# Optimization experiments

Hardware: AMD Instinct MI355X
Metric: run time of the kernel (lower is better)

The kernel has to match this reference:

```python
import jax, jax.numpy as jnp
import numpy as np

K = 4096
N = 11008
GROUP_SIZE = 128
NUM_GROUPS = K // GROUP_SIZE
BATCH = 4
SEQ = 2048


def setup_inputs() -> dict:
    key = jax.random.key(0)
    kx, kw, ks = jax.random.split(key, 3)
    x = jax.random.normal(kx, (BATCH, SEQ, K), dtype=jnp.float16)
    # packed uint8 bytes, each holding two INT4 values (stored as int32)
    weight_packed = jax.random.randint(kw, (N, K // 2), 0, 256, dtype=jnp.int32)
    # positive group-wise scales ~ abs(randn)*0.1 -> uniform*0.1 is fine statistically
    scales = (jax.random.uniform(ks, (N, NUM_GROUPS), dtype=jnp.float32) * 0.1).astype(jnp.float16)
    return {"x": x, "weight_packed": weight_packed, "scales": scales}


def _dequantize(weight_packed, scales):
    # unpack: low nibble first, then high nibble -> (N, K) values in [0, 15]
    low = weight_packed & 15
    high = (weight_packed >> 4) & 15
    w_int = jnp.stack([low, high], axis=-1).reshape(weight_packed.shape[0], -1)  # (N, K)
    # symmetric dequant with implicit zero-point 8, group-wise scales
    scales_expanded = jnp.repeat(scales, GROUP_SIZE, axis=1)  # (N, K)
    return scales_expanded * (w_int.astype(jnp.float16) - jnp.float16(8.0))


def reference(x, weight_packed, scales):
    # Y = X @ W_dequant.T : (B, S, K) x (N, K) -> (B, S, N)
    w_dequant = _dequantize(weight_packed, scales)  # (N, K) fp16
    out = jnp.einsum('bsk,nk->bsn', x, w_dequant)
    return out.astype(jnp.float16)
```

## Files before the change

kernel.cpp:

```cpp
#include <hip/hip_runtime.h>
#include <stdint.h>


namespace {

typedef unsigned int u32;
typedef unsigned short u16;
typedef __attribute__((ext_vector_type(8))) short bf16x8;
typedef __attribute__((ext_vector_type(4))) float f32x4;
typedef __attribute__((ext_vector_type(4))) u32 u32x4;

constexpr int Mt = 8192;
constexpr int Nt = 11008;
constexpr int Kt = 4096;
constexpr int KP = Kt / 2;
constexpr int NG = 32;
constexpr int BM = 256;
constexpr int BN = 128;
constexpr int BK = 64;
constexpr int THREADS = 512;
constexpr int GRID = (Mt / BM) * (Nt / BN);
constexpr int NKT = Kt / BK;
constexpr int NB_CNT = Nt / BN;

__device__ __forceinline__ u16 f2bf(float f) {
  u32 u = __float_as_uint(f);
  return (u16)((u + 0x7FFFu + ((u >> 16) & 1u)) >> 16);
}
__device__ __forceinline__ u32 pk2bf(float a, float b) {
  return (u32)f2bf(a) | ((u32)f2bf(b) << 16);
}
__device__ __forceinline__ u32 dqpair(u32 b, float s, float c) {
  float f0 = (float)(b & 15u);
  float f1 = (float)((b >> 4) & 15u);
  return pk2bf(fmaf(f0, s, c), fmaf(f1, s, c));
}
__device__ __forceinline__ void async16(const void* g, void* l) {
  __builtin_amdgcn_global_load_lds(
      (const __attribute__((address_space(1))) u32*)g,
      (__attribute__((address_space(3))) u32*)l, 16, 0, 0);
}

__global__ __launch_bounds__(256) void cvt_x(const float* __restrict__ X,
                                             u32* __restrict__ O) {
  const int total = Mt * Kt / 4;
  for (int j = blockIdx.x * 256 + threadIdx.x; j < total;
       j += (int)(gridDim.x * 256)) {
    float4 v = ((const float4*)X)[j];
    ((uint2*)O)[j] = make_uint2(pk2bf(v.x, v.y), pk2bf(v.z, v.w));
  }
}

__global__ __launch_bounds__(256) void cvt_w(const int* __restrict__ W,
                                             const float* __restrict__ S,
                                             u32* __restrict__ O) {
  const int total = Nt * KP / 4;
  for (int j = blockIdx.x * 256 + threadIdx.x; j < total;
       j += (int)(gridDim.x * 256)) {
    int4 v = ((const int4*)W)[j];
    int vv[4] = {v.x, v.y, v.z, v.w};
    const int j0 = j * 4;
    const int row = j0 >> 11;
    const int jj = j0 & 2047;
    const float* sr = S + (size_t)row * NG;
    u32x4 o;
    #pragma unroll
    for (int e = 0; e < 4; ++e) {
      float s = sr[(jj + e) >> 6];
      o[e] = dqpair((u32)vv[e], s, -8.f * s);
    }
    ((u32x4*)O)[j] = o;
  }
}

template <bool PRE>
__global__ __launch_bounds__(THREADS) void gemm(
    const float* __restrict__ Xf, const int* __restrict__ W,
    const float* __restrict__ S, const u16* __restrict__ Xb,
    const u16* __restrict__ Wb, float* __restrict__ Y) {
  __shared__ __align__(16) unsigned char Alds[BM * BK * 2];
  __shared__ __align__(16) unsigned char Blds[BN * BK * 2];

  const int tid = (int)threadIdx.x;
  const int lane = tid & 63;
  const int wid = tid >> 6;
  const int wm = wid >> 1;
  const int wn = wid & 1;

  const int bid = (int)blockIdx.x;
  const int wg = (bid & 7) * (GRID / 8) + (bid >> 3);
  const int mb = wg / NB_CNT;
  const int nb = wg - mb * NB_CNT;
  const int m0 = mb * BM;
  const int n0 = nb * BN;

  const int frow = lane & 15;
  const int fk = lane >> 4;
  const int fswz = (lane & 7) << 4;
  const unsigned char* aRd = Alds + (wm * 64 + frow) * 128;
  const unsigned char* bRd = Blds + (wn * 64 + frow) * 128;

  f32x4 acc[4][4];
  #pragma unroll
  for (int i = 0; i < 4; ++i)
    #pragma unroll
    for (int j = 0; j < 4; ++j) acc[i][j] = f32x4{0.f, 0.f, 0.f, 0.f};

  const int lrow = lane >> 3, lslot = lane & 7;
  const int psl = lslot ^ (lrow & 7);
  const u16* aG = PRE ? Xb + (size_t)(m0 + wid * 32 + lrow) * Kt + psl * 8 : nullptr;
  const u16* bG = PRE ? Wb + (size_t)(n0 + wid * 16 + lrow) * Kt + psl * 8 : nullptr;
  unsigned char* aL = Alds + (wid * 32) * 128;
  unsigned char* bL = Blds + (wid * 16) * 128;

  const int arow = tid >> 3, acol = tid & 7;
  const float* fA = PRE ? nullptr : Xf + (size_t)(m0 + arow) * Kt + acol * 8;
  unsigned char* fAD = Alds + arow * 128 + ((acol ^ (arow & 7)) << 4);
  const int nloc = tid >> 3, c4 = tid & 7;
  const int* fB0 = PRE ? nullptr : W + (size_t)(n0 + nloc) * KP + c4 * 4;
  const int* fB1 = PRE ? nullptr : fB0 + (size_t)64 * KP;
  const float* sp0 = PRE ? nullptr : S + (size_t)(n0 + nloc) * NG;
  const float* sp1 = PRE ? nullptr : sp0 + (size_t)64 * NG;
  unsigned char* fBD0 = Blds + nloc * 128 + ((c4 ^ (nloc & 7)) << 4);
  unsigned char* fBD1 = fBD0 + 64 * 128;

  #pragma unroll 1
  for (int kt = 0; kt < NKT; ++kt) {
    const int k0 = kt * BK;

    if constexpr (PRE) {
      #pragma unroll
      for (int i = 0; i < 4; ++i) async16(aG + (size_t)i * 8 * Kt + k0, aL + i * 1024);
      #pragma unroll
      for (int j = 0; j < 2; ++j) async16(bG + (size_t)j * 8 * Kt + k0, bL + j * 1024);
    } else {
      #pragma unroll
      for (int p = 0; p < 4; ++p) {
        float4 x0 = *(const float4*)(fA + (size_t)p * 64 * Kt + k0);
        float4 x1 = *(const float4*)(fA + (size_t)p * 64 * Kt + k0 + 4);
        u32x4 q;
        q[0] = pk2bf(x0.x, x0.y); q[1] = pk2bf(x0.z, x0.w);
        q[2] = pk2bf(x1.x, x1.y); q[3] = pk2bf(x1.z, x1.w);
        *(u32x4*)(fAD + p * 64 * 128) = q;
      }
      const int g = k0 >> 7;
      const float s0 = sp0[g], s1 = sp1[g];
      const float c0 = -8.f * s0, c1 = -8.f * s1;
      const int4 w0 = *(const int4*)(fB0 + (k0 >> 1));
      const int4 w1 = *(const int4*)(fB1 + (k0 >> 1));
      u32x4 q0, q1;
      q0[0] = dqpair((u32)w0.x, s0, c0); q0[1] = dqpair((u32)w0.y, s0, c0);
      q0[2] = dqpair((u32)w0.z, s0, c0); q0[3] = dqpair((u32)w0.w, s0, c0);
      q1[0] = dqpair((u32)w1.x, s1, c1); q1[1] = dqpair((u32)w1.y, s1, c1);
      q1[2] = dqpair((u32)w1.z, s1, c1); q1[3] = dqpair((u32)w1.w, s1, c1);
      *(u32x4*)fBD0 = q0;
      *(u32x4*)fBD1 = q1;
    }

    __syncthreads();

    #pragma unroll
    for (int kk = 0; kk < 2; ++kk) {
      const int koff = (kk * 64 + fk * 16) ^ fswz;
      bf16x8 af[4], bfr[4];
      #pragma unroll
      for (int fm = 0; fm < 4; ++fm)
        af[fm] = *(const bf16x8*)(aRd + fm * 16 * 128 + koff);
      #pragma unroll
      for (int fn = 0; fn < 4; ++fn)
        bfr[fn] = *(const bf16x8*)(bRd + fn * 16 * 128 + koff);
      #pragma unroll
      for (int fm = 0; fm < 4; ++fm)
        #pragma unroll
        for (int fn = 0; fn < 4; ++fn)
          acc[fm][fn] = __builtin_amdgcn_mfma_f32_16x16x32_bf16(
              af[fm], bfr[fn], acc[fm][fn], 0, 0, 0);
    }

    __syncthreads();
  }

  #pragma unroll
  for (int fm = 0; fm < 4; ++fm) {
    #pragma unroll
    for (int r = 0; r < 4; ++r) {
      const size_t mrow = (size_t)(m0 + wm * 64 + fm * 16 + fk * 4 + r) * Nt;
      #pragma unroll
      for (int fn = 0; fn < 4; ++fn) {
        Y[mrow + (size_t)(n0 + wn * 64 + fn * 16 + frow)] = acc[fm][fn][r];
      }
    }
  }
}

}

extern "C" void kernel_launch(void* const* d_in, const int* in_sizes, int n_in,
                              void* d_out, int out_size, void* d_ws, size_t ws_size,
                              hipStream_t stream) {
  (void)in_sizes; (void)n_in; (void)out_size;
  const float* X = (const float*)d_in[0];
  const int* W   = (const int*)d_in[1];
  const float* S = (const float*)d_in[2];
  float* Y       = (float*)d_out;

  const size_t xbytes = (size_t)Mt * Kt * 2;
  const size_t wbytes = (size_t)Nt * Kt * 2;

  if (ws_size >= xbytes + wbytes) {
    u16* Xb = (u16*)d_ws;
    u16* Wb = (u16*)((char*)d_ws + xbytes);
    cvt_x<<<dim3(2048), dim3(256), 0, stream>>>(X, (u32*)Xb);
    cvt_w<<<dim3(2048), dim3(256), 0, stream>>>(W, S, (u32*)Wb);
    gemm<true><<<dim3(GRID), dim3(THREADS), 0, stream>>>(nullptr, nullptr, nullptr,
                                                         Xb, Wb, Y);
  } else {
    gemm<false><<<dim3(GRID), dim3(THREADS), 0, stream>>>(X, W, S, nullptr, nullptr, Y);
  }
}
```

Baseline: 761.6 us.

## Double-buffer async LDS loads with 256x256 tiles in pre-converted GEMM

Splits the templated GEMM into a pre-converted path and a fused fallback. The pre-converted path now uses 256x256 output tiles, so each wave computes 8x4 MFMA fragments. It prefetches the next K-slice into a second LDS buffer with async global-to-LDS loads and waits with explicit vmcnt/s_barrier instead of __syncthreads. It also raises wave priority around the MFMA block. The aim is to overlap global loads with compute and improve operand reuse. The cost is 128KB of LDS and a doubled accumulator footprint, and __launch_bounds__(512,2) may force register spills.

```diff
diff --git a/kernel.cpp b/kernel.cpp
--- a/kernel.cpp
+++ b/kernel.cpp
@@ -16,12 +16,13 @@
 constexpr int KP = Kt / 2;
 constexpr int NG = 32;
 constexpr int BM = 256;
-constexpr int BN = 128;
+constexpr int BN = 256;
 constexpr int BK = 64;
 constexpr int THREADS = 512;
 constexpr int GRID = (Mt / BM) * (Nt / BN);
 constexpr int NKT = Kt / BK;
 constexpr int NB_CNT = Nt / BN;
+constexpr int TILE_BYTES = BM * BK * 2;
 
 __device__ __forceinline__ u16 f2bf(float f) {
   u32 u = __float_as_uint(f);
@@ -73,13 +74,114 @@
   }
 }
 
-template <bool PRE>
-__global__ __launch_bounds__(THREADS) void gemm(
+__global__ __launch_bounds__(THREADS, 2) void gemm_pre(
+    const u16* __restrict__ Xb, const u16* __restrict__ Wb,
+    float* __restrict__ Y) {
+  __shared__ __align__(16) unsigned char smem[4 * TILE_BYTES];
+
+  const int tid  = (int)threadIdx.x;
+  const int lane = tid & 63;
+  const int wid  = tid >> 6;
+  const int wm   = wid >> 2;
+  const int wn   = wid & 3;
+
+  const int bid = (int)blockIdx.x;
+  const int wg  = (bid & 7) * (GRID / 8) + (bid >> 3);
+  const int mb  = wg / NB_CNT;
+  const int nb  = wg - mb * NB_CNT;
+  const int m0  = mb * BM;
+  const int n0  = nb * BN;
+
+  const int lrow = lane >> 3;
+  const int psl  = (lane & 7) ^ lrow;
+  const u16* aG = Xb + (size_t)(m0 + wid * 32 + lrow) * Kt + psl * 8;
+  const u16* bG = Wb + (size_t)(n0 + wid * 32 + lrow) * Kt + psl * 8;
+  const int ldsW = wid * 4096;
+
+  const int frow = lane & 15;
+  const int fk   = lane >> 4;
+  const int fswz = (lane & 7) << 4;
+  const int aRdOff = (wm * 128 + frow) * 128;
+  const int bRdOff = (wn * 64 + frow) * 128;
+
+  f32x4 acc[8][4];
+  #pragma unroll
+  for (int i = 0; i < 8; ++i)
+    #pragma unroll
+    for (int j = 0; j < 4; ++j) acc[i][j] = f32x4{0.f, 0.f, 0.f, 0.f};
+
+  #define STAGE(b, kt)                                                        \
+    do {                                                                      \
+      unsigned char* aL = smem + (b) * 2 * TILE_BYTES + ldsW;                 \
+      unsigned char* bL = aL + TILE_BYTES;                                    \
+      const int koff_ = (kt) * BK;                                            \
+      _Pragma("unroll")                                                       \
+      for (int i_ = 0; i_ < 4; ++i_) {                                        \
+        async16(aG + (size_t)i_ * 8 * Kt + koff_, aL + i_ * 1024);            \
+        async16(bG + (size_t)i_ * 8 * Kt + koff_, bL + i_ * 1024);            \
+      }                                                                       \
+    } while (0)
+
+  STAGE(0, 0);
+
+  #pragma unroll 1
+  for (int kt = 0; kt < NKT; ++kt) {
+    const int cur = kt & 1;
+    if (kt + 1 < NKT) {
+      STAGE(cur ^ 1, kt + 1);
+      asm volatile("s_waitcnt vmcnt(8)" ::: "memory");
+    } else {
+      asm volatile("s_waitcnt vmcnt(0)" ::: "memory");
+    }
+    asm volatile("s_barrier" ::: "memory");
+
+    const unsigned char* aRd = smem + cur * 2 * TILE_BYTES + aRdOff;
+    const unsigned char* bRd = aRd + TILE_BYTES - aRdOff + bRdOff;
+
+    #pragma unroll
+    for (int kk = 0; kk < 2; ++kk) {
+      const int koff = (kk * 64 + fk * 16) ^ fswz;
+      bf16x8 af[8], bfr[4];
+      #pragma unroll
+      for (int fm = 0; fm < 8; ++fm)
+        af[fm] = *(const bf16x8*)(aRd + fm * 16 * 128 + koff);
+      #pragma unroll
+      for (int fn = 0; fn < 4; ++fn)
+        bfr[fn] = *(const bf16x8*)(bRd + fn * 16 * 128 + koff);
+      __builtin_amdgcn_s_setprio(1);
+      #pragma unroll
+      for (int fm = 0; fm < 8; ++fm)
+        #pragma unroll
+        for (int fn = 0; fn < 4; ++fn)
+          acc[fm][fn] = __builtin_amdgcn_mfma_f32_16x16x32_bf16(
+              af[fm], bfr[fn], acc[fm][fn], 0, 0, 0);
+      __builtin_amdgcn_s_setprio(0);
+    }
+
+    asm volatile("s_barrier" ::: "memory");
+  }
+  #undef STAGE
+
+  #pragma unroll
+  for (int fm = 0; fm < 8; ++fm) {
+    #pragma unroll
+    for (int r = 0; r < 4; ++r) {
+      const size_t mrow = (size_t)(m0 + wm * 128 + fm * 16 + fk * 4 + r) * Nt;
+      #pragma unroll
+      for (int fn = 0; fn < 4; ++fn) {
+        Y[mrow + (size_t)(n0 + wn * 64 + fn * 16 + frow)] = acc[fm][fn][r];
+      }
+    }
+  }
+}
+
+__global__ __launch_bounds__(THREADS) void gemm_fused(
     const float* __restrict__ Xf, const int* __restrict__ W,
-    const float* __restrict__ S, const u16* __restrict__ Xb,
-    const u16* __restrict__ Wb, float* __restrict__ Y) {
+    const float* __restrict__ S, float* __restrict__ Y) {
+  constexpr int FBN = 128;
+  constexpr int FGRID_NB = Nt / FBN;
   __shared__ __align__(16) unsigned char Alds[BM * BK * 2];
-  __shared__ __align__(16) unsigned char Blds[BN * BK * 2];
+  __shared__ __align__(16) unsigned char Blds[FBN * BK * 2];
 
   const int tid = (int)threadIdx.x;
   const int lane = tid & 63;
@@ -88,11 +190,12 @@
   const int wn = wid & 1;
 
   const int bid = (int)blockIdx.x;
-  const int wg = (bid & 7) * (GRID / 8) + (bid >> 3);
-  const int mb = wg / NB_CNT;
-  const int nb = wg - mb * NB_CNT;
+  const int fgrid = (Mt / BM) * FGRID_NB;
+  const int wg = (bid & 7) * (fgrid / 8) + (bid >> 3);
+  const int mb = wg / FGRID_NB;
+  const int nb = wg - mb * FGRID_NB;
   const int m0 = mb * BM;
-  const int n0 = nb * BN;
+  const int n0 = nb * FBN;
 
   const int frow = lane & 15;
   const int fk = lane >> 4;
@@ -106,56 +209,41 @@
     #pragma unroll
     for (int j = 0; j < 4; ++j) acc[i][j] = f32x4{0.f, 0.f, 0.f, 0.f};
 
-  const int lrow = lane >> 3, lslot = lane & 7;
-  const int psl = lslot ^ (lrow & 7);
-  const u16* aG = PRE ? Xb + (size_t)(m0 + wid * 32 + lrow) * Kt + psl * 8 : nullptr;
-  const u16* bG = PRE ? Wb + (size_t)(n0 + wid * 16 + lrow) * Kt + psl * 8 : nullptr;
-  unsigned char* aL = Alds + (wid * 32) * 128;
-  unsigned char* bL = Blds + (wid * 16) * 128;
-
   const int arow = tid >> 3, acol = tid & 7;
-  const float* fA = PRE ? nullptr : Xf + (size_t)(m0 + arow) * Kt + acol * 8;
+  const float* fA = Xf + (size_t)(m0 + arow) * Kt + acol * 8;
   unsigned char* fAD = Alds + arow * 128 + ((acol ^ (arow & 7)) << 4);
   const int nloc = tid >> 3, c4 = tid & 7;
-  const int* fB0 = PRE ? nullptr : W + (size_t)(n0 + nloc) * KP + c4 * 4;
-  const int* fB1 = PRE ? nullptr : fB0 + (size_t)64 * KP;
-  const float* sp0 = PRE ? nullptr : S + (size_t)(n0 + nloc) * NG;
-  const float* sp1 = PRE ? nullptr : sp0 + (size_t)64 * NG;
+  const int* fB0 = W + (size_t)(n0 + nloc) * KP + c4 * 4;
+  const int* fB1 = fB0 + (size_t)64 * KP;
+  const float* sp0 = S + (size_t)(n0 + nloc) * NG;
+  const float* sp1 = sp0 + (size_t)64 * NG;
   unsigned char* fBD0 = Blds + nloc * 128 + ((c4 ^ (nloc & 7)) << 4);
   unsigned char* fBD1 = fBD0 + 64 * 128;
 
   #pragma unroll 1
   for (int kt = 0; kt < NKT; ++kt) {
     const int k0 = kt * BK;
-
-    if constexpr (PRE) {
-      #pragma unroll
-      for (int i = 0; i < 4; ++i) async16(aG + (size_t)i * 8 * Kt + k0, aL + i * 1024);
-      #pragma unroll
-      for (int j = 0; j < 2; ++j) async16(bG + (size_t)j * 8 * Kt + k0, bL + j * 1024);
-    } else {
-      #pragma unroll
-      for (int p = 0; p < 4; ++p) {
-        float4 x0 = *(const float4*)(fA + (size_t)p * 64 * Kt + k0);
-        float4 x1 = *(const float4*)(fA + (size_t)p * 64 * Kt + k0 + 4);
-        u32x4 q;
-        q[0] = pk2bf(x0.x, x0.y); q[1] = pk2bf(x0.z, x0.w);
-        q[2] = pk2bf(x1.x, x1.y); q[3] = pk2bf(x1.z, x1.w);
-        *(u32x4*)(fAD + p * 64 * 128) = q;
-      }
-      const int g = k0 >> 7;
-      const float s0 = sp0[g], s1 = sp1[g];
-      const float c0 = -8.f * s0, c1 = -8.f * s1;
-      const int4 w0 = *(const int4*)(fB0 + (k0 >> 1));
-      const int4 w1 = *(const int4*)(fB1 + (k0 >> 1));
-      u32x4 q0, q1;
-      q0[0] = dqpair((u32)w0.x, s0, c0); q0[1] = dqpair((u32)w0.y, s0, c0);
-      q0[2] = dqpair((u32)w0.z, s0, c0); q0[3] = dqpair((u32)w0.w, s0, c0);
-      q1[0] = dqpair((u32)w1.x, s1, c1); q1[1] = dqpair((u32)w1.y, s1, c1);
-      q1[2] = dqpair((u32)w1.z, s1, c1); q1[3] = dqpair((u32)w1.w, s1, c1);
-      *(u32x4*)fBD0 = q0;
-      *(u32x4*)fBD1 = q1;
-    }
+    #pragma unroll
+    for (int p = 0; p < 4; ++p) {
+      float4 x0 = *(const float4*)(fA + (size_t)p * 64 * Kt + k0);
+      float4 x1 = *(const float4*)(fA + (size_t)p * 64 * Kt + k0 + 4);
+      u32x4 q;
+      q[0] = pk2bf(x0.x, x0.y); q[1] = pk2bf(x0.z, x0.w);
+      q[2] = pk2bf(x1.x, x1.y); q[3] = pk2bf(x1.z, x1.w);
+      *(u32x4*)(fAD + p * 64 * 128) = q;
+    }
+    const int g = k0 >> 7;
+    const float s0 = sp0[g], s1 = sp1[g];
+    const float c0 = -8.f * s0, c1 = -8.f * s1;
+    const int4 w0 = *(const int4*)(fB0 + (k0 >> 1));
+    const int4 w1 = *(const int4*)(fB1 + (k0 >> 1));
+    u32x4 q0, q1;
+    q0[0] = dqpair((u32)w0.x, s0, c0); q0[1] = dqpair((u32)w0.y, s0, c0);
+    q0[2] = dqpair((u32)w0.z, s0, c0); q0[3] = dqpair((u32)w0.w, s0, c0);
+    q1[0] = dqpair((u32)w1.x, s1, c1); q1[1] = dqpair((u32)w1.y, s1, c1);
+    q1[2] = dqpair((u32)w1.z, s1, c1); q1[3] = dqpair((u32)w1.w, s1, c1);
+    *(u32x4*)fBD0 = q0;
+    *(u32x4*)fBD1 = q1;
 
     __syncthreads();
 
@@ -176,7 +264,6 @@
           acc[fm][fn] = __builtin_amdgcn_mfma_f32_16x16x32_bf16(
               af[fm], bfr[fn], acc[fm][fn], 0, 0, 0);
     }
-
     __syncthreads();
   }
 
@@ -186,9 +273,8 @@
     for (int r = 0; r < 4; ++r) {
       const size_t mrow = (size_t)(m0 + wm * 64 + fm * 16 + fk * 4 + r) * Nt;
       #pragma unroll
-      for (int fn = 0; fn < 4; ++fn) {
+      for (int fn = 0; fn < 4; ++fn)
         Y[mrow + (size_t)(n0 + wn * 64 + fn * 16 + frow)] = acc[fm][fn][r];
-      }
     }
   }
 }
@@ -212,9 +298,8 @@
     u16* Wb = (u16*)((char*)d_ws + xbytes);
     cvt_x<<<dim3(2048), dim3(256), 0, stream>>>(X, (u32*)Xb);
     cvt_w<<<dim3(2048), dim3(256), 0, stream>>>(W, S, (u32*)Wb);
-    gemm<true><<<dim3(GRID), dim3(THREADS), 0, stream>>>(nullptr, nullptr, nullptr,
-                                                         Xb, Wb, Y);
+    gemm_pre<<<dim3(GRID), dim3(THREADS), 0, stream>>>(Xb, Wb, Y);
   } else {
-    gemm<false><<<dim3(GRID), dim3(THREADS), 0, stream>>>(X, W, S, nullptr, nullptr, Y);
-  }
-}
+    gemm_fused<<<dim3((Mt / BM) * (Nt / 128)), dim3(THREADS), 0, stream>>>(X, W, S, Y);
+  }
+}
```

Result: slower. 805.1 us (+5.7%).

## Triple-buffer LDS with async prefetch two tiles ahead in pre-converted GEMM

Applied to the files above, without the earlier changes.

Splits the workspace GEMM path into its own kernel that halves the K tile and keeps three LDS slots, issuing async global-to-LDS loads two iterations ahead. Explicit vmcnt waits and raw barriers replace the synchronous load-then-sync pattern, and MFMA sections are wrapped in raised wave priority. The goal is to hide global load latency behind matrix math instead of stalling every iteration. In exchange it adds more barriers per unit of K work and a new swizzle pattern that could cause LDS bank conflicts.

```diff
diff --git a/kernel.cpp b/kernel.cpp
--- a/kernel.cpp
+++ b/kernel.cpp
@@ -17,11 +17,12 @@
 constexpr int NG = 32;
 constexpr int BM = 256;
 constexpr int BN = 128;
-constexpr int BK = 64;
+constexpr int BK = 32;
 constexpr int THREADS = 512;
 constexpr int GRID = (Mt / BM) * (Nt / BN);
 constexpr int NKT = Kt / BK;
 constexpr int NB_CNT = Nt / BN;
+constexpr int SLOT_BYTES = (BM + BN) * BK * 2;
 
 __device__ __forceinline__ u16 f2bf(float f) {
   u32 u = __float_as_uint(f);
@@ -73,13 +74,117 @@
   }
 }
 
-template <bool PRE>
-__global__ __launch_bounds__(THREADS) void gemm(
+__global__ __launch_bounds__(THREADS) void gemm_pre(
+    const u16* __restrict__ Xb, const u16* __restrict__ Wb,
+    float* __restrict__ Y) {
+  __shared__ __align__(16) unsigned char smem[3 * SLOT_BYTES];
+
+  const int tid  = (int)threadIdx.x;
+  const int lane = tid & 63;
+  const int wid  = tid >> 6;
+  const int wm   = wid >> 1;
+  const int wn   = wid & 1;
+
+  const int bid = (int)blockIdx.x;
+  const int wg  = (bid & 7) * (GRID / 8) + (bid >> 3);
+  const int mb  = wg / NB_CNT;
+  const int nb  = wg - mb * NB_CNT;
+  const int m0  = mb * BM;
+  const int n0  = nb * BN;
+
+  const int srow = tid >> 2;
+  const int sswz = (tid & 3) ^ (srow & 3);
+  const u16* aG0 = Xb + (size_t)(m0 + srow) * Kt + sswz * 8;
+  const u16* aG1 = aG0 + (size_t)128 * Kt;
+  const u16* bG  = Wb + (size_t)(n0 + srow) * Kt + sswz * 8;
+  const int ldst = tid * 16;
+
+  const int frow = lane & 15;
+  const int fk   = lane >> 4;
+  const int rswz = ((lane >> 4) ^ (lane & 3)) << 4;
+  const int aOff = (wm * 64 + frow) * 64 + rswz;
+  const int bOff = 16384 + (wn * 64 + frow) * 64 + rswz;
+
+  f32x4 acc[4][4];
+  #pragma unroll
+  for (int i = 0; i < 4; ++i)
+    #pragma unroll
+    for (int j = 0; j < 4; ++j) acc[i][j] = f32x4{0.f, 0.f, 0.f, 0.f};
+
+  #define STAGE(slot, kt)                                                     \
+    do {                                                                      \
+      unsigned char* base_ = smem + (slot) * SLOT_BYTES;                      \
+      const int k0_ = (kt) * BK;                                              \
+      async16(aG0 + k0_, base_ + ldst);                                       \
+      async16(aG1 + k0_, base_ + 8192 + ldst);                                \
+      async16(bG + k0_, base_ + 16384 + ldst);                                \
+    } while (0)
+
+  #define COMPUTE(slot)                                                      \
+    do {                                                                     \
+      const unsigned char* base_ = smem + (slot) * SLOT_BYTES;               \
+      bf16x8 af[4], bfr[4];                                                  \
+      _Pragma("unroll")                                                      \
+      for (int fm = 0; fm < 4; ++fm)                                         \
+        af[fm] = *(const bf16x8*)(base_ + aOff + fm * 1024);                 \
+      _Pragma("unroll")                                                      \
+      for (int fn = 0; fn < 4; ++fn)                                         \
+        bfr[fn] = *(const bf16x8*)(base_ + bOff + fn * 1024);                \
+      __builtin_amdgcn_s_setprio(1);                                         \
+      _Pragma("unroll")                                                      \
+      for (int fm = 0; fm < 4; ++fm)                                         \
+        _Pragma("unroll")                                                    \
+        for (int fn = 0; fn < 4; ++fn)                                       \
+          acc[fm][fn] = __builtin_amdgcn_mfma_f32_16x16x32_bf16(             \
+              af[fm], bfr[fn], acc[fm][fn], 0, 0, 0);                        \
+      __builtin_amdgcn_s_setprio(0);                                         \
+    } while (0)
+
+  STAGE(0, 0);
+  STAGE(1, 1);
+
+  int cur = 0, st = 2;
+  #pragma unroll 1
+  for (int t = 0; t < NKT - 2; ++t) {
+    STAGE(st, t + 2);
+    asm volatile("s_waitcnt vmcnt(6)" ::: "memory");
+    asm volatile("s_barrier" ::: "memory");
+    COMPUTE(cur);
+    asm volatile("s_barrier" ::: "memory");
+    cur = (cur == 2) ? 0 : cur + 1;
+    st  = (st == 2) ? 0 : st + 1;
+  }
+  asm volatile("s_waitcnt vmcnt(3)" ::: "memory");
+  asm volatile("s_barrier" ::: "memory");
+  COMPUTE(cur);
+  asm volatile("s_barrier" ::: "memory");
+  cur = (cur == 2) ? 0 : cur + 1;
+  asm volatile("s_waitcnt vmcnt(0)" ::: "memory");
+  asm volatile("s_barrier" ::: "memory");
+  COMPUTE(cur);
+  #undef STAGE
+  #undef COMPUTE
+
+  #pragma unroll
+  for (int fm = 0; fm < 4; ++fm) {
+    #pragma unroll
+    for (int r = 0; r < 4; ++r) {
+      const size_t mrow = (size_t)(m0 + wm * 64 + fm * 16 + fk * 4 + r) * Nt;
+      #pragma unroll
+      for (int fn = 0; fn < 4; ++fn) {
+        Y[mrow + (size_t)(n0 + wn * 64 + fn * 16 + frow)] = acc[fm][fn][r];
+      }
+    }
+  }
+}
+
+__global__ __launch_bounds__(THREADS) void gemm_fused(
     const float* __restrict__ Xf, const int* __restrict__ W,
-    const float* __restrict__ S, const u16* __restrict__ Xb,
-    const u16* __restrict__ Wb, float* __restrict__ Y) {
-  __shared__ __align__(16) unsigned char Alds[BM * BK * 2];
-  __shared__ __align__(16) unsigned char Blds[BN * BK * 2];
+    const float* __restrict__ S, float* __restrict__ Y) {
+  constexpr int FBK = 64;
+  constexpr int FNKT = Kt / FBK;
+  __shared__ __align__(16) unsigned char Alds[BM * FBK * 2];
+  __shared__ __align__(16) unsigned char Blds[BN * FBK * 2];
 
   const int tid = (int)threadIdx.x;
   const int lane = tid & 63;
@@ -106,56 +211,41 @@
     #pragma unroll
     for (int j = 0; j < 4; ++j) acc[i][j] = f32x4{0.f, 0.f, 0.f, 0.f};
 
-  const int lrow = lane >> 3, lslot = lane & 7;
-  const int psl = lslot ^ (lrow & 7);
-  const u16* aG = PRE ? Xb + (size_t)(m0 + wid * 32 + lrow) * Kt + psl * 8 : nullptr;
-  const u16* bG = PRE ? Wb + (size_t)(n0 + wid * 16 + lrow) * Kt + psl * 8 : nullptr;
-  unsigned char* aL = Alds + (wid * 32) * 128;
-  unsigned char* bL = Blds + (wid * 16) * 128;
-
   const int arow = tid >> 3, acol = tid & 7;
-  const float* fA = PRE ? nullptr : Xf + (size_t)(m0 + arow) * Kt + acol * 8;
+  const float* fA = Xf + (size_t)(m0 + arow) * Kt + acol * 8;
   unsigned char* fAD = Alds + arow * 128 + ((acol ^ (arow & 7)) << 4);
   const int nloc = tid >> 3, c4 = tid & 7;
-  const int* fB0 = PRE ? nullptr : W + (size_t)(n0 + nloc) * KP + c4 * 4;
-  const int* fB1 = PRE ? nullptr : fB0 + (size_t)64 * KP;
-  const float* sp0 = PRE ? nullptr : S + (size_t)(n0 + nloc) * NG;
-  const float* sp1 = PRE ? nullptr : sp0 + (size_t)64 * NG;
+  const int* fB0 = W + (size_t)(n0 + nloc) * KP + c4 * 4;
+  const int* fB1 = fB0 + (size_t)64 * KP;
+  const float* sp0 = S + (size_t)(n0 + nloc) * NG;
+  const float* sp1 = sp0 + (size_t)64 * NG;
   unsigned char* fBD0 = Blds + nloc * 128 + ((c4 ^ (nloc & 7)) << 4);
   unsigned char* fBD1 = fBD0 + 64 * 128;
 
   #pragma unroll 1
-  for (int kt = 0; kt < NKT; ++kt) {
-    const int k0 = kt * BK;
-
-    if constexpr (PRE) {
-      #pragma unroll
-      for (int i = 0; i < 4; ++i) async16(aG + (size_t)i * 8 * Kt + k0, aL + i * 1024);
-      #pragma unroll
-      for (int j = 0; j < 2; ++j) async16(bG + (size_t)j * 8 * Kt + k0, bL + j * 1024);
-    } else {
-      #pragma unroll
-      for (int p = 0; p < 4; ++p) {
-        float4 x0 = *(const float4*)(fA + (size_t)p * 64 * Kt + k0);
-        float4 x1 = *(const float4*)(fA + (size_t)p * 64 * Kt + k0 + 4);
-        u32x4 q;
-        q[0] = pk2bf(x0.x, x0.y); q[1] = pk2bf(x0.z, x0.w);
-        q[2] = pk2bf(x1.x, x1.y); q[3] = pk2bf(x1.z, x1.w);
-        *(u32x4*)(fAD + p * 64 * 128) = q;
-      }
-      const int g = k0 >> 7;
-      const float s0 = sp0[g], s1 = sp1[g];
-      const float c0 = -8.f * s0, c1 = -8.f * s1;
-      const int4 w0 = *(const int4*)(fB0 + (k0 >> 1));
-      const int4 w1 = *(const int4*)(fB1 + (k0 >> 1));
-      u32x4 q0, q1;
-      q0[0] = dqpair((u32)w0.x, s0, c0); q0[1] = dqpair((u32)w0.y, s0, c0);
-      q0[2] = dqpair((u32)w0.z, s0, c0); q0[3] = dqpair((u32)w0.w, s0, c0);
-      q1[0] = dqpair((u32)w1.x, s1, c1); q1[1] = dqpair((u32)w1.y, s1, c1);
-      q1[2] = dqpair((u32)w1.z, s1, c1); q1[3] = dqpair((u32)w1.w, s1, c1);
-      *(u32x4*)fBD0 = q0;
-      *(u32x4*)fBD1 = q1;
-    }
+  for (int kt = 0; kt < FNKT; ++kt) {
+    const int k0 = kt * FBK;
+    #pragma unroll
+    for (int p = 0; p < 4; ++p) {
+      float4 x0 = *(const float4*)(fA + (size_t)p * 64 * Kt + k0);
+      float4 x1 = *(const float4*)(fA + (size_t)p * 64 * Kt + k0 + 4);
+      u32x4 q;
+      q[0] = pk2bf(x0.x, x0.y); q[1] = pk2bf(x0.z, x0.w);
+      q[2] = pk2bf(x1.x, x1.y); q[3] = pk2bf(x1.z, x1.w);
+      *(u32x4*)(fAD + p * 64 * 128) = q;
+    }
+    const int g = k0 >> 7;
+    const float s0 = sp0[g], s1 = sp1[g];
+    const float c0 = -8.f * s0, c1 = -8.f * s1;
+    const int4 w0 = *(const int4*)(fB0 + (k0 >> 1));
+    const int4 w1 = *(const int4*)(fB1 + (k0 >> 1));
+    u32x4 q0, q1;
+    q0[0] = dqpair((u32)w0.x, s0, c0); q0[1] = dqpair((u32)w0.y, s0, c0);
+    q0[2] = dqpair((u32)w0.z, s0, c0); q0[3] = dqpair((u32)w0.w, s0, c0);
+    q1[0] = dqpair((u32)w1.x, s1, c1); q1[1] = dqpair((u32)w1.y, s1, c1);
+    q1[2] = dqpair((u32)w1.z, s1, c1); q1[3] = dqpair((u32)w1.w, s1, c1);
+    *(u32x4*)fBD0 = q0;
+    *(u32x4*)fBD1 = q1;
 
     __syncthreads();
 
@@ -176,7 +266,6 @@
           acc[fm][fn] = __builtin_amdgcn_mfma_f32_16x16x32_bf16(
               af[fm], bfr[fn], acc[fm][fn], 0, 0, 0);
     }
-
     __syncthreads();
   }
 
@@ -186,9 +275,8 @@
     for (int r = 0; r < 4; ++r) {
       const size_t mrow = (size_t)(m0 + wm * 64 + fm * 16 + fk * 4 + r) * Nt;
       #pragma unroll
-      for (int fn = 0; fn < 4; ++fn) {
+      for (int fn = 0; fn < 4; ++fn)
         Y[mrow + (size_t)(n0 + wn * 64 + fn * 16 + frow)] = acc[fm][fn][r];
-      }
     }
   }
 }
@@ -212,9 +300,8 @@
     u16* Wb = (u16*)((char*)d_ws + xbytes);
     cvt_x<<<dim3(2048), dim3(256), 0, stream>>>(X, (u32*)Xb);
     cvt_w<<<dim3(2048), dim3(256), 0, stream>>>(W, S, (u32*)Wb);
-    gemm<true><<<dim3(GRID), dim3(THREADS), 0, stream>>>(nullptr, nullptr, nullptr,
-                                                         Xb, Wb, Y);
+    gemm_pre<<<dim3(GRID), dim3(THREADS), 0, stream>>>(Xb, Wb, Y);
   } else {
-    gemm<false><<<dim3(GRID), dim3(THREADS), 0, stream>>>(X, W, S, nullptr, nullptr, Y);
-  }
-}
+    gemm_fused<<<dim3(GRID), dim3(THREADS), 0, stream>>>(X, W, S, Y);
+  }
+}
```

Result: slower. 808.6 us (+6.2%).
